# Kernel optimization log

Measured on AMD Instinct MI355X. Metric: run time of the kernel, lower is better.

## Reference

```python
import jax, jax.numpy as jnp
import numpy as np

B, N, D, H = 4, 1024, 1024, 16
DH = D // H
MLP = 4 * D
EPS = 1e-6


def setup_inputs() -> dict:
    key = jax.random.key(0)
    ks = jax.random.split(key, 16)
    s = lambda fan_in: 1.0 / np.sqrt(fan_in)
    inp = {
        "x": jax.random.normal(ks[0], (B, N, D), jnp.float32),
        "c": jax.random.normal(ks[1], (B, D), jnp.float32),
        # weights stored (in, out); torch Linear is x @ W.T + b
        "Wq": jax.random.normal(ks[2], (D, D), jnp.float32) * s(D),
        "bq": jnp.zeros((D,), jnp.float32),
        "Wkv": jax.random.normal(ks[3], (D, 2 * D), jnp.float32) * s(D),
        "bkv": jnp.zeros((2 * D,), jnp.float32),
        "Wo": jax.random.normal(ks[4], (D, D), jnp.float32) * s(D),
        "bo": jnp.zeros((D,), jnp.float32),
        "W1": jax.random.normal(ks[5], (D, MLP), jnp.float32) * s(D),
        "b1": jnp.zeros((MLP,), jnp.float32),
        "W2": jax.random.normal(ks[6], (MLP, D), jnp.float32) * s(MLP),
        "b2": jnp.zeros((D,), jnp.float32),
        "Wada": jax.random.normal(ks[7], (D, 6 * D), jnp.float32) * s(D),
        "bada": jnp.zeros((6 * D,), jnp.float32),
    }
    return inp


def _layernorm(h):
    mu = jnp.mean(h, axis=-1, keepdims=True)
    var = jnp.mean(jnp.square(h - mu), axis=-1, keepdims=True)
    return (h - mu) / jnp.sqrt(var + EPS)


def _modulate(h, shift, scale):
    return h * (1.0 + scale[:, None, :]) + shift[:, None, :]


def reference(x, c, Wq, bq, Wkv, bkv, Wo, bo, W1, b1, W2, b2, Wada, bada):
    scale = DH ** -0.5
    mod = jax.nn.silu(c) @ Wada + bada  # [B, 6D]
    sh_msa, sc_msa, g_msa, sh_mlp, sc_mlp, g_mlp = jnp.split(mod, 6, axis=-1)

    # --- attention branch ---
    h = _modulate(_layernorm(x), sh_msa, sc_msa)
    q = (h @ Wq + bq).reshape(B, N, H, DH)
    kv = h @ Wkv + bkv
    k, v = jnp.split(kv, 2, axis=-1)
    k = k.reshape(B, N, H, DH)
    v = v.reshape(B, N, H, DH)
    sim = jnp.einsum("bihd,bjhd->bhij", q, k) * scale  # [B,H,N,N]
    attn = jax.nn.softmax(sim, axis=-1)
    out = jnp.einsum("bhij,bjhd->bihd", attn, v).reshape(B, N, D)
    out = out @ Wo + bo
    x = x + g_msa[:, None, :] * out

    # --- MLP branch ---
    h2 = _modulate(_layernorm(x), sh_mlp, sc_mlp)
    m = jax.nn.gelu(h2 @ W1 + b1, approximate=True) @ W2 + b2
    x = x + g_mlp[:, None, :] * m
    return x
```

## Files before the change

kernel.cpp:

```cpp
#include <hip/hip_runtime.h>
#include <hip/hip_bf16.h>
#include <cstdint>

typedef __attribute__((ext_vector_type(4))) float f32x4;
typedef __attribute__((ext_vector_type(16))) float f32x16;
typedef __attribute__((ext_vector_type(8))) short s16x8;
typedef __attribute__((ext_vector_type(4))) unsigned u32x4;
typedef unsigned short u16;

#define B_  4
#define N_  1024
#define D_  1024
#define H_  16
#define DH_ 64
#define M_  4096
#define SIXD 6144

#define WAITV(n) asm volatile("s_waitcnt vmcnt(" #n ")" ::: "memory")

__device__ __forceinline__ u16 f2bf(float f) {
    unsigned u = __builtin_bit_cast(unsigned, f);
    unsigned r = (u + 0x7fffu + ((u >> 16) & 1u)) >> 16;
    return (u16)r;
}

__device__ __forceinline__ unsigned cvtpk(float a, float b) {
    unsigned r;
    asm("v_cvt_pk_bf16_f32 %0, %1, %2" : "=v"(r) : "v"(a), "v"(b));
    return r;
}

__device__ __forceinline__ void gload16(const void* g, void* l) {
    __builtin_amdgcn_global_load_lds((const __attribute__((address_space(1))) void*)g,
                                     (__attribute__((address_space(3))) void*)l,
                                     16, 0, 0);
}

__global__ __launch_bounds__(256) void prep_all(const float* __restrict__ Wq,
                                                const float* __restrict__ Wkv,
                                                const float* __restrict__ Wo,
                                                const float* __restrict__ W1,
                                                const float* __restrict__ W2,
                                                const float* __restrict__ c,
                                                const float* __restrict__ Wada,
                                                const float* __restrict__ bada,
                                                u16* __restrict__ wqkvT,
                                                u16* __restrict__ woT,
                                                u16* __restrict__ w1T,
                                                u16* __restrict__ w2T,
                                                float* __restrict__ mod) {
    int id = blockIdx.x;
    int tid = threadIdx.x;
    if (id >= 12288) {
        __shared__ float sc[D_];
        int mb = id - 12288;
        int b = mb / 24;
        int col = (mb % 24) * 256 + tid;
        for (int i = tid; i < D_; i += 256) {
            float v = c[b * D_ + i];
            sc[i] = v / (1.f + __expf(-v));
        }
        __syncthreads();
        float a0 = 0.f, a1 = 0.f, a2 = 0.f, a3 = 0.f;
        for (int k = 0; k < D_; k += 4) {
            a0 = fmaf(sc[k + 0], Wada[(size_t)(k + 0) * SIXD + col], a0);
            a1 = fmaf(sc[k + 1], Wada[(size_t)(k + 1) * SIXD + col], a1);
            a2 = fmaf(sc[k + 2], Wada[(size_t)(k + 2) * SIXD + col], a2);
            a3 = fmaf(sc[k + 3], Wada[(size_t)(k + 3) * SIXD + col], a3);
        }
        mod[b * SIXD + col] = bada[col] + ((a0 + a1) + (a2 + a3));
        return;
    }
    const float* in; u16* outp; int R, C, loc;
    if (id < 1024)      { in = Wq;  outp = wqkvT;           R = 1024; C = 1024; loc = id; }
    else if (id < 3072) { in = Wkv; outp = wqkvT + 1048576; R = 1024; C = 2048; loc = id - 1024; }
    else if (id < 4096) { in = Wo;  outp = woT;             R = 1024; C = 1024; loc = id - 3072; }
    else if (id < 8192) { in = W1;  outp = w1T;             R = 1024; C = 4096; loc = id - 4096; }
    else                { in = W2;  outp = w2T;             R = 4096; C = 1024; loc = id - 8192; }
    int tpc = C >> 5;
    int bx = loc % tpc, by = loc / tpc;
    __shared__ float t[32][33];
    int tx = tid & 31, ty = tid >> 5;
    int r0 = by * 32, c0 = bx * 32;
#pragma unroll
    for (int i = 0; i < 4; ++i)
        t[ty + 8 * i][tx] = in[(size_t)(r0 + ty + 8 * i) * C + c0 + tx];
    __syncthreads();
#pragma unroll
    for (int i = 0; i < 4; ++i)
        outp[(size_t)(c0 + ty + 8 * i) * R + r0 + tx] = f2bf(t[tx][ty + 8 * i]);
}

__global__ __launch_bounds__(256) void ln_mod(const float* __restrict__ x,
                                              const float* __restrict__ mod,
                                              int shift_c, int scale_c,
                                              u16* __restrict__ h) {
    int row = blockIdx.x;
    int b = row >> 10;
    int tid = threadIdx.x, w = tid >> 6;
    float4 xv = ((const float4*)(x + (size_t)row * D_))[tid];
    float s  = xv.x + xv.y + xv.z + xv.w;
    float s2 = xv.x * xv.x + xv.y * xv.y + xv.z * xv.z + xv.w * xv.w;
#pragma unroll
    for (int m = 1; m <= 32; m <<= 1) { s += __shfl_xor(s, m); s2 += __shfl_xor(s2, m); }
    __shared__ float red[8];
    if ((tid & 63) == 0) { red[w * 2] = s; red[w * 2 + 1] = s2; }
    __syncthreads();
    float S  = red[0] + red[2] + red[4] + red[6];
    float S2 = red[1] + red[3] + red[5] + red[7];
    float mu = S * (1.f / D_);
    float var = S2 * (1.f / D_) - mu * mu;
    float rstd = rsqrtf(var + 1e-6f);
    int d0 = tid * 4;
    float4 shv = *(const float4*)(mod + b * SIXD + shift_c * D_ + d0);
    float4 scv = *(const float4*)(mod + b * SIXD + scale_c * D_ + d0);
    ushort4 o;
    o.x = f2bf((xv.x - mu) * rstd * (1.f + scv.x) + shv.x);
    o.y = f2bf((xv.y - mu) * rstd * (1.f + scv.y) + shv.y);
    o.z = f2bf((xv.z - mu) * rstd * (1.f + scv.z) + shv.z);
    o.w = f2bf((xv.w - mu) * rstd * (1.f + scv.w) + shv.w);
    *(ushort4*)(h + (size_t)row * D_ + d0) = o;
}

__global__ __launch_bounds__(256) void gemm_qkv(const u16* __restrict__ A,
                                                const u16* __restrict__ Bt,
                                                const float* __restrict__ bias,
                                                const float* __restrict__ bias2,
                                                u16* __restrict__ out,
                                                int M, int Nn, int K) {
    __shared__ char lds[2][32768];
    const int tid = threadIdx.x;
    const int w = tid >> 6, lane = tid & 63;
    const int li = lane & 15, lg = lane >> 4;
    const int nwg = gridDim.x * gridDim.y;
    const int flat = blockIdx.y * gridDim.x + blockIdx.x;
    const int wg = (flat & 7) * (nwg >> 3) + (flat >> 3);
    const int m0 = (wg / gridDim.x) * 128, n0 = (wg % gridDim.x) * 128;
    const int wr = w >> 1, wc = w & 1;

    f32x4 acc[4][4];
#pragma unroll
    for (int i = 0; i < 4; ++i)
#pragma unroll
        for (int j = 0; j < 4; ++j) acc[i][j] = (f32x4){0.f, 0.f, 0.f, 0.f};

    auto STAGE = [&](int kk, char* buf) {
#pragma unroll
        for (int j = 0; j < 8; ++j) {
            int basec = j * 256 + w * 64;
            int idx = basec + lane;
            int idl = idx & 1023;
            int row = idl >> 3, cc = idl & 7;
            const u16* src;
            if (idx < 1024)
                src = A + (size_t)(m0 + row) * K + kk + ((cc ^ (row & 7)) << 3);
            else
                src = Bt + (size_t)(n0 + row) * K + kk + ((cc ^ (row & 7)) << 3);
            gload16(src, buf + basec * 16);
        }
    };

    const int nt = K >> 6;
    STAGE(0, lds[0]);
    __syncthreads();
    int cur = 0;
    for (int t = 0; t < nt; ++t) {
        if (t + 1 < nt) { STAGE((t + 1) << 6, lds[cur ^ 1]); WAITV(8); }
        else WAITV(0);
        __builtin_amdgcn_s_barrier();
        __builtin_amdgcn_sched_barrier(0);
        const char* Ab = lds[cur];
        const char* Bb = lds[cur] + 16384;
#pragma unroll
        for (int hh = 0; hh < 2; ++hh) {
            s16x8 af[4], bfr[4];
#pragma unroll
            for (int mi = 0; mi < 4; ++mi) {
                int r = wr * 64 + mi * 16 + li;
                af[mi] = *(const s16x8*)(Ab + r * 128 + (((hh * 4 + lg) ^ (r & 7)) << 4));
            }
#pragma unroll
            for (int nj = 0; nj < 4; ++nj) {
                int r = wc * 64 + nj * 16 + li;
                bfr[nj] = *(const s16x8*)(Bb + r * 128 + (((hh * 4 + lg) ^ (r & 7)) << 4));
            }
#pragma unroll
            for (int mi = 0; mi < 4; ++mi)
#pragma unroll
                for (int nj = 0; nj < 4; ++nj)
                    acc[mi][nj] = __builtin_amdgcn_mfma_f32_16x16x32_bf16(
                        af[mi], bfr[nj], acc[mi][nj], 0, 0, 0);
        }
        __builtin_amdgcn_s_barrier();
        cur ^= 1;
    }

#pragma unroll
    for (int mi = 0; mi < 4; ++mi) {
#pragma unroll
        for (int nj = 0; nj < 4; ++nj) {
            int col = n0 + wc * 64 + nj * 16 + li;
            float bv = (col < D_) ? bias[col] : bias2[col - D_];
#pragma unroll
            for (int rg = 0; rg < 4; ++rg) {
                int grow = m0 + wr * 64 + mi * 16 + 4 * lg + rg;
                float v = acc[mi][nj][rg] + bv;
                int b = grow >> 10, n = grow & 1023;
                if (col < D_) {
                    int hd = col >> 6, dh = col & 63;
                    out[(((size_t)(b * H_ + hd)) * N_ + n) * DH_ + dh] = f2bf(v);
                } else if (col < 2 * D_) {
                    int c2 = col - D_;
                    int hd = c2 >> 6, dh = c2 & 63;
                    out[4194304u + (((size_t)(b * H_ + hd)) * N_ + n) * DH_ + dh] = f2bf(v);
                } else {
                    int c2 = col - 2 * D_;
                    int hd = c2 >> 6, dh = c2 & 63;
                    out[8388608u + (((size_t)(b * H_ + hd)) * DH_ + dh) * N_ + n] = f2bf(v);
                }
            }
        }
    }
}

template <int EPI>
__global__ __launch_bounds__(256) void gemm_bt(const u16* __restrict__ A,
                                               const u16* __restrict__ Bt,
                                               const float* __restrict__ bias,
                                               void* __restrict__ out,
                                               const float* __restrict__ xres,
                                               const float* __restrict__ mod,
                                               int M, int Nn, int K, int gate_c) {
    __shared__ char lds[2][32768];
    const int tid = threadIdx.x;
    const int w = tid >> 6, lane = tid & 63;
    const int li = lane & 15, lg = lane >> 4;
    const int nwg = gridDim.x * gridDim.y;
    const int flat = blockIdx.y * gridDim.x + blockIdx.x;
    const int wg = (flat & 7) * (nwg >> 3) + (flat >> 3);
    const int m0 = (wg / gridDim.x) * 128, n0 = (wg % gridDim.x) * 128;
    const int wr = w >> 1, wc = w & 1;

    f32x4 acc[4][4];
#pragma unroll
    for (int i = 0; i < 4; ++i)
#pragma unroll
        for (int j = 0; j < 4; ++j) acc[i][j] = (f32x4){0.f, 0.f, 0.f, 0.f};

    auto STAGE = [&](int kk, char* buf) {
#pragma unroll
        for (int j = 0; j < 8; ++j) {
            int basec = j * 256 + w * 64;
            int idx = basec + lane;
            int idl = idx & 1023;
            int row = idl >> 3, cc = idl & 7;
            const u16* src;
            if (idx < 1024)
                src = A + (size_t)(m0 + row) * K + kk + ((cc ^ (row & 7)) << 3);
            else
                src = Bt + (size_t)(n0 + row) * K + kk + ((cc ^ (row & 7)) << 3);
            gload16(src, buf + basec * 16);
        }
    };

    const int nt = K >> 6;
    STAGE(0, lds[0]);
    __syncthreads();
    int cur = 0;
    for (int t = 0; t < nt; ++t) {
        if (t + 1 < nt) { STAGE((t + 1) << 6, lds[cur ^ 1]); WAITV(8); }
        else WAITV(0);
        __builtin_amdgcn_s_barrier();
        __builtin_amdgcn_sched_barrier(0);
        const char* Ab = lds[cur];
        const char* Bb = lds[cur] + 16384;
#pragma unroll
        for (int hh = 0; hh < 2; ++hh) {
            s16x8 af[4], bfr[4];
#pragma unroll
            for (int mi = 0; mi < 4; ++mi) {
                int r = wr * 64 + mi * 16 + li;
                af[mi] = *(const s16x8*)(Ab + r * 128 + (((hh * 4 + lg) ^ (r & 7)) << 4));
            }
#pragma unroll
            for (int nj = 0; nj < 4; ++nj) {
                int r = wc * 64 + nj * 16 + li;
                bfr[nj] = *(const s16x8*)(Bb + r * 128 + (((hh * 4 + lg) ^ (r & 7)) << 4));
            }
#pragma unroll
            for (int mi = 0; mi < 4; ++mi)
#pragma unroll
                for (int nj = 0; nj < 4; ++nj)
                    acc[mi][nj] = __builtin_amdgcn_mfma_f32_16x16x32_bf16(
                        af[mi], bfr[nj], acc[mi][nj], 0, 0, 0);
        }
        __builtin_amdgcn_s_barrier();
        cur ^= 1;
    }

#pragma unroll
    for (int mi = 0; mi < 4; ++mi) {
#pragma unroll
        for (int nj = 0; nj < 4; ++nj) {
            int col = n0 + wc * 64 + nj * 16 + li;
            float bv = bias[col];
#pragma unroll
            for (int rg = 0; rg < 4; ++rg) {
                int grow = m0 + wr * 64 + mi * 16 + 4 * lg + rg;
                float v = acc[mi][nj][rg] + bv;
                int b = grow >> 10;
                size_t off = (size_t)grow * D_ + col;
                float g = mod[b * SIXD + gate_c * D_ + col];
                ((float*)out)[off] = xres[off] + g * v;
            }
        }
    }
}

__global__ __launch_bounds__(512, 2) void gemm256_gelu(const u16* __restrict__ A,
                                                       const u16* __restrict__ Bt,
                                                       const float* __restrict__ bias,
                                                       u16* __restrict__ out,
                                                       int M, int Nn, int K) {
    __shared__ char lds[2][65536];
    const int tid = threadIdx.x;
    const int w = tid >> 6, lane = tid & 63;
    const int li = lane & 15, lg = lane >> 4;
    const int wr = w >> 1, wc = w & 1;

    const int flat = blockIdx.x;
    const int wg = (flat & 7) * 32 + (flat >> 3);
    const int mg = wg >> 6, r_ = wg & 63;
    const int mt = mg * 4 + (r_ & 3), nt_ = r_ >> 2;
    const int m0 = mt * 256, n0 = nt_ * 256;

    f32x4 acc[4][8];
#pragma unroll
    for (int i = 0; i < 4; ++i)
#pragma unroll
        for (int j = 0; j < 8; ++j) acc[i][j] = (f32x4){0.f, 0.f, 0.f, 0.f};

    auto STAGE = [&](int kk, char* buf) {
#pragma unroll
        for (int j = 0; j < 4; ++j) {
            int basec = j * 512 + w * 64;
            int idx = basec + lane;
            int row = idx >> 3, cc = idx & 7;
            gload16(A + (size_t)(m0 + row) * K + kk + ((cc ^ (row & 7)) << 3),
                    buf + basec * 16);
            gload16(Bt + (size_t)(n0 + row) * K + kk + ((cc ^ (row & 7)) << 3),
                    buf + 32768 + basec * 16);
        }
    };

    const int nt = K >> 6;
    STAGE(0, lds[0]);
    __syncthreads();
    int cur = 0;
    for (int t = 0; t < nt; ++t) {
        if (t + 1 < nt) STAGE((t + 1) << 6, lds[cur ^ 1]);
        const char* Ab = lds[cur];
        const char* Bb = lds[cur] + 32768;
#pragma unroll
        for (int hh = 0; hh < 2; ++hh) {
            s16x8 af[4], bfr[8];
#pragma unroll
            for (int mi = 0; mi < 4; ++mi) {
                int r = wr * 64 + mi * 16 + li;
                af[mi] = *(const s16x8*)(Ab + r * 128 + (((hh * 4 + lg) ^ (r & 7)) << 4));
            }
#pragma unroll
            for (int nj = 0; nj < 8; ++nj) {
                int r = wc * 128 + nj * 16 + li;
                bfr[nj] = *(const s16x8*)(Bb + r * 128 + (((hh * 4 + lg) ^ (r & 7)) << 4));
            }
#pragma unroll
            for (int mi = 0; mi < 4; ++mi)
#pragma unroll
                for (int nj = 0; nj < 8; ++nj)
                    acc[mi][nj] = __builtin_amdgcn_mfma_f32_16x16x32_bf16(
                        af[mi], bfr[nj], acc[mi][nj], 0, 0, 0);
        }
        __syncthreads();
        cur ^= 1;
    }

#pragma unroll
    for (int nj = 0; nj < 8; ++nj) {
        int col = n0 + wc * 128 + nj * 16 + li;
        float bv = bias[col];
#pragma unroll
        for (int mi = 0; mi < 4; ++mi) {
#pragma unroll
            for (int rg = 0; rg < 4; ++rg) {
                int grow = m0 + wr * 64 + mi * 16 + 4 * lg + rg;
                float v = acc[mi][nj][rg] + bv;
                float u = 0.7978845608028654f * v * (1.f + 0.044715f * v * v);
                u = fminf(fmaxf(u, -15.f), 15.f);
                float e = __expf(2.f * u);
                float th = (e - 1.f) / (e + 1.f);
                out[(size_t)grow * (size_t)Nn + col] = f2bf(0.5f * v * (1.f + th));
            }
        }
    }
}

__global__ __launch_bounds__(256) void attn2(const u16* __restrict__ q,
                                             const u16* __restrict__ k,
                                             const u16* __restrict__ vt,
                                             u16* __restrict__ o) {
    __shared__ __align__(16) char qs[16384];
    __shared__ __align__(16) char kv[2][16384];
    const int tid = threadIdx.x, w = tid >> 6, lane = tid & 63;
    const int l31 = lane & 31, hi = lane >> 5;
    const int flat = blockIdx.x;
    const int wgs = (flat & 7) * 64 + (flat >> 3);
    const int bh = wgs >> 3, qt = wgs & 7;
    const size_t base = (size_t)bh * (N_ * DH_);
    const int q0 = qt * 128;

#pragma unroll
    for (int j = 0; j < 4; ++j) {
        int basec = j * 256 + w * 64;
        int idx = basec + lane;
        int row = idx >> 3, cc = idx & 7;
        gload16(q + base + (size_t)(q0 + row) * DH_ + ((cc ^ (row & 7)) << 3),
                qs + basec * 16);
    }
    auto STAGEKV = [&](int t, char* buf) {
#pragma unroll
        for (int j = 0; j < 4; ++j) {
            int basec = j * 256 + w * 64;
            int idx = basec + lane;
            if (idx < 512) {
                int row = idx >> 3, cc = idx & 7;
                gload16(k + base + (size_t)(t * 64 + row) * DH_ + ((cc ^ (row & 7)) << 3),
                        buf + basec * 16);
            } else {
                int i2 = idx - 512;
                int row = i2 >> 3, cc = i2 & 7;
                gload16(vt + base + (size_t)row * N_ + t * 64 + ((cc ^ (row & 7)) << 3),
                        buf + basec * 16);
            }
        }
    };
    STAGEKV(0, kv[0]);
    __syncthreads();

    s16x8 qf[4];
    const int qr = w * 32 + l31;
#pragma unroll
    for (int st = 0; st < 4; ++st)
        qf[st] = *(const s16x8*)(qs + qr * 128 + (((st * 2 + hi) ^ (qr & 7)) << 4));

    f32x16 oa[2];
#pragma unroll
    for (int r = 0; r < 16; ++r) { oa[0][r] = 0.f; oa[1][r] = 0.f; }
    float mrow = -3e38f, lrow = 0.f;
    const float CSC = 0.125f * 1.44269504088896f;

    int cur = 0;
    for (int t = 0; t < 16; ++t) {
        if (t + 1 < 16) STAGEKV(t + 1, kv[cur ^ 1]);
        const char* Kb = kv[cur];
        const char* Vb = kv[cur] + 8192;

        f32x16 s[2];
#pragma unroll
        for (int r = 0; r < 16; ++r) { s[0][r] = 0.f; s[1][r] = 0.f; }
#pragma unroll
        for (int st = 0; st < 4; ++st) {
#pragma unroll
            for (int ks = 0; ks < 2; ++ks) {
                int r = ks * 32 + l31;
                s16x8 ka = *(const s16x8*)(Kb + r * 128 + (((st * 2 + hi) ^ (r & 7)) << 4));
                s[ks] = __builtin_amdgcn_mfma_f32_32x32x16_bf16(ka, qf[st], s[ks], 0, 0, 0);
            }
        }

        float tmax = s[0][0];
#pragma unroll
        for (int r = 1; r < 16; ++r) tmax = fmaxf(tmax, s[0][r]);
#pragma unroll
        for (int r = 0; r < 16; ++r) tmax = fmaxf(tmax, s[1][r]);
        tmax = fmaxf(tmax, __shfl_xor(tmax, 32));
        float mn = fmaxf(mrow, tmax);
        float al = __builtin_amdgcn_exp2f((mrow - mn) * CSC);
        float nmc = -mn * CSC;
        float rs0 = 0.f, rs1 = 0.f;
#pragma unroll
        for (int r = 0; r < 16; ++r) {
            float p0 = __builtin_amdgcn_exp2f(fmaf(s[0][r], CSC, nmc));
            float p1 = __builtin_amdgcn_exp2f(fmaf(s[1][r], CSC, nmc));
            s[0][r] = p0; s[1][r] = p1;
            rs0 += p0; rs1 += p1;
        }
        float rs = rs0 + rs1;
        rs += __shfl_xor(rs, 32);
        lrow = lrow * al + rs;
        mrow = mn;
#pragma unroll
        for (int r = 0; r < 16; ++r) { oa[0][r] *= al; oa[1][r] *= al; }

        unsigned u[16];
#pragma unroll
        for (int ks = 0; ks < 2; ++ks)
#pragma unroll
            for (int j = 0; j < 4; ++j) {
                u[ks * 8 + 2 * j]     = cvtpk(s[ks][4 * j + 0], s[ks][4 * j + 1]);
                u[ks * 8 + 2 * j + 1] = cvtpk(s[ks][4 * j + 2], s[ks][4 * j + 3]);
            }

#pragma unroll
        for (int kstep = 0; kstep < 4; ++kstep) {
            unsigned b0 = u[kstep * 4 + 0], b1 = u[kstep * 4 + 1];
            unsigned b2 = u[kstep * 4 + 2], b3 = u[kstep * 4 + 3];
            asm volatile("v_permlane32_swap_b32 %0, %1" : "+v"(b0), "+v"(b2));
            asm volatile("v_permlane32_swap_b32 %0, %1" : "+v"(b1), "+v"(b3));
            u32x4 pbu = (u32x4){b0, b1, b2, b3};
            s16x8 pb = __builtin_bit_cast(s16x8, pbu);
#pragma unroll
            for (int ds = 0; ds < 2; ++ds) {
                int r = ds * 32 + l31;
                s16x8 va = *(const s16x8*)(Vb + r * 128 + (((kstep * 2 + hi) ^ (r & 7)) << 4));
                oa[ds] = __builtin_amdgcn_mfma_f32_32x32x16_bf16(va, pb, oa[ds], 0, 0, 0);
            }
        }
        __syncthreads();
        cur ^= 1;
    }

    float inv = 1.f / lrow;
#pragma unroll
    for (int ds = 0; ds < 2; ++ds)
#pragma unroll
        for (int j = 0; j < 4; ++j)
#pragma unroll
            for (int t2 = 0; t2 < 2; ++t2) {
                unsigned pk = cvtpk(oa[ds][4 * j + 2 * t2] * inv,
                                    oa[ds][4 * j + 2 * t2 + 1] * inv);
                int row = qr;
                int dch = 4 * ds + j;
                *(unsigned*)(qs + row * 128 + ((dch ^ (row & 7)) << 4) +
                             (4 * hi + 2 * t2) * 2) = pk;
            }
    __syncthreads();
    {
        int r = tid >> 1, h2 = tid & 1;
        const int b = bh >> 4, hd = bh & 15;
        size_t obase = ((size_t)(b * N_ + q0 + r)) * D_ + hd * DH_;
#pragma unroll
        for (int c = 0; c < 4; ++c) {
            int c2 = h2 * 4 + c;
            s16x8 v = *(const s16x8*)(qs + r * 128 + ((c2 ^ (r & 7)) << 4));
            *(s16x8*)(o + obase + c2 * 8) = v;
        }
    }
}

extern "C" void kernel_launch(void* const* d_in, const int* in_sizes, int n_in,
                              void* d_out, int out_size, void* d_ws, size_t ws_size,
                              hipStream_t stream) {
    const float* x    = (const float*)d_in[0];
    const float* c    = (const float*)d_in[1];
    const float* Wq   = (const float*)d_in[2];
    const float* bq   = (const float*)d_in[3];
    const float* Wkv  = (const float*)d_in[4];
    const float* bkv  = (const float*)d_in[5];
    const float* Wo   = (const float*)d_in[6];
    const float* bo   = (const float*)d_in[7];
    const float* W1   = (const float*)d_in[8];
    const float* b1   = (const float*)d_in[9];
    const float* W2   = (const float*)d_in[10];
    const float* b2   = (const float*)d_in[11];
    const float* Wada = (const float*)d_in[12];
    const float* bada = (const float*)d_in[13];

    char* ws = (char*)d_ws;
    const size_t MB = 1024 * 1024;
    u16*   wqkvT = (u16*)(ws + 0);
    u16*   woT  = (u16*)(ws + 6 * MB);
    u16*   w1T  = (u16*)(ws + 8 * MB);
    u16*   w2T  = (u16*)(ws + 16 * MB);
    float* mod  = (float*)(ws + 24 * MB);
    u16*   h    = (u16*)(ws + 25 * MB);
    u16*   qb   = (u16*)(ws + 33 * MB);
    u16*   ao   = (u16*)(ws + 57 * MB);
    float* x1   = (float*)(ws + 65 * MB);
    u16*   m1   = (u16*)(ws + 33 * MB);
    float* outp = (float*)d_out;

    prep_all<<<12384, 256, 0, stream>>>(Wq, Wkv, Wo, W1, W2, c, Wada, bada,
                                        wqkvT, woT, w1T, w2T, mod);

    ln_mod<<<M_, 256, 0, stream>>>(x, mod, 0, 1, h);

    gemm_qkv<<<dim3(24, 32), 256, 0, stream>>>(h, wqkvT, bq, bkv, qb, M_, 3 * D_, D_);

    attn2<<<512, 256, 0, stream>>>(qb, qb + 4194304, qb + 8388608, ao);

    gemm_bt<2><<<dim3(8, 32), 256, 0, stream>>>(ao, woT, bo, x1, x, mod, M_, D_, D_, 2);

    ln_mod<<<M_, 256, 0, stream>>>(x1, mod, 3, 4, h);

    gemm256_gelu<<<256, 512, 0, stream>>>(h, w1T, b1, m1, M_, 4 * D_, D_);
    gemm_bt<4><<<dim3(8, 32), 256, 0, stream>>>(m1, w2T, b2, outp, x1, mod, M_, D_, 4 * D_, 5);
}
```

Measured before the change: 242.0 us.

## Split adaLN modulation GEMV over K and enlarge weight transpose tiles

```diff
diff --git a/kernel.cpp b/kernel.cpp
--- a/kernel.cpp
+++ b/kernel.cpp
@@ -43,52 +43,69 @@
                                                 const float* __restrict__ W2,
                                                 const float* __restrict__ c,
                                                 const float* __restrict__ Wada,
-                                                const float* __restrict__ bada,
                                                 u16* __restrict__ wqkvT,
                                                 u16* __restrict__ woT,
                                                 u16* __restrict__ w1T,
                                                 u16* __restrict__ w2T,
-                                                float* __restrict__ mod) {
+                                                float* __restrict__ modp) {
     int id = blockIdx.x;
     int tid = threadIdx.x;
-    if (id >= 12288) {
-        __shared__ float sc[D_];
-        int mb = id - 12288;
-        int b = mb / 24;
-        int col = (mb % 24) * 256 + tid;
-        for (int i = tid; i < D_; i += 256) {
-            float v = c[b * D_ + i];
-            sc[i] = v / (1.f + __expf(-v));
+    if (id < 768) {
+        __shared__ float sc[128];
+        int colblk = id % 24, b = (id / 24) & 3, ks = id / 96;
+        int col = colblk * 256 + tid;
+        int k0 = ks * 128;
+        if (tid < 128) {
+            float v = c[b * D_ + k0 + tid];
+            sc[tid] = v / (1.f + __expf(-v));
         }
         __syncthreads();
         float a0 = 0.f, a1 = 0.f, a2 = 0.f, a3 = 0.f;
-        for (int k = 0; k < D_; k += 4) {
-            a0 = fmaf(sc[k + 0], Wada[(size_t)(k + 0) * SIXD + col], a0);
-            a1 = fmaf(sc[k + 1], Wada[(size_t)(k + 1) * SIXD + col], a1);
-            a2 = fmaf(sc[k + 2], Wada[(size_t)(k + 2) * SIXD + col], a2);
-            a3 = fmaf(sc[k + 3], Wada[(size_t)(k + 3) * SIXD + col], a3);
-        }
-        mod[b * SIXD + col] = bada[col] + ((a0 + a1) + (a2 + a3));
+#pragma unroll 4
+        for (int k = 0; k < 128; k += 4) {
+            a0 = fmaf(sc[k + 0], Wada[(size_t)(k0 + k + 0) * SIXD + col], a0);
+            a1 = fmaf(sc[k + 1], Wada[(size_t)(k0 + k + 1) * SIXD + col], a1);
+            a2 = fmaf(sc[k + 2], Wada[(size_t)(k0 + k + 2) * SIXD + col], a2);
+            a3 = fmaf(sc[k + 3], Wada[(size_t)(k0 + k + 3) * SIXD + col], a3);
+        }
+        modp[(size_t)(ks * 4 + b) * SIXD + col] = (a0 + a1) + (a2 + a3);
         return;
     }
+    int t_ = id - 768;
     const float* in; u16* outp; int R, C, loc;
-    if (id < 1024)      { in = Wq;  outp = wqkvT;           R = 1024; C = 1024; loc = id; }
-    else if (id < 3072) { in = Wkv; outp = wqkvT + 1048576; R = 1024; C = 2048; loc = id - 1024; }
-    else if (id < 4096) { in = Wo;  outp = woT;             R = 1024; C = 1024; loc = id - 3072; }
-    else if (id < 8192) { in = W1;  outp = w1T;             R = 1024; C = 4096; loc = id - 4096; }
-    else                { in = W2;  outp = w2T;             R = 4096; C = 1024; loc = id - 8192; }
-    int tpc = C >> 5;
+    if (t_ < 256)       { in = Wq;  outp = wqkvT;           R = 1024; C = 1024; loc = t_; }
+    else if (t_ < 768)  { in = Wkv; outp = wqkvT + 1048576; R = 1024; C = 2048; loc = t_ - 256; }
+    else if (t_ < 1024) { in = Wo;  outp = woT;             R = 1024; C = 1024; loc = t_ - 768; }
+    else if (t_ < 2048) { in = W1;  outp = w1T;             R = 1024; C = 4096; loc = t_ - 1024; }
+    else                { in = W2;  outp = w2T;             R = 4096; C = 1024; loc = t_ - 2048; }
+    int tpc = C >> 6;
     int bx = loc % tpc, by = loc / tpc;
-    __shared__ float t[32][33];
-    int tx = tid & 31, ty = tid >> 5;
-    int r0 = by * 32, c0 = bx * 32;
-#pragma unroll
-    for (int i = 0; i < 4; ++i)
-        t[ty + 8 * i][tx] = in[(size_t)(r0 + ty + 8 * i) * C + c0 + tx];
+    __shared__ float t[64][65];
+    int r0 = by * 64, c0 = bx * 64;
+    int cx = tid & 63, ry = tid >> 6;
+#pragma unroll
+    for (int i = 0; i < 16; ++i) {
+        int rr = ry + 4 * i;
+        t[rr][cx] = in[(size_t)(r0 + rr) * C + c0 + cx];
+    }
     __syncthreads();
 #pragma unroll
-    for (int i = 0; i < 4; ++i)
-        outp[(size_t)(c0 + ty + 8 * i) * R + r0 + tx] = f2bf(t[tx][ty + 8 * i]);
+    for (int i = 0; i < 16; ++i) {
+        int cc = ry + 4 * i;
+        outp[(size_t)(c0 + cc) * R + r0 + cx] = f2bf(t[cx][cc]);
+    }
+}
+
+__global__ __launch_bounds__(256) void reduce_mod(const float* __restrict__ modp,
+                                                  const float* __restrict__ bada,
+                                                  float* __restrict__ mod) {
+    int col = blockIdx.x * 256 + threadIdx.x;
+    int b = blockIdx.y;
+    float s = bada[col];
+#pragma unroll
+    for (int ks = 0; ks < 8; ++ks)
+        s += modp[(size_t)(ks * 4 + b) * SIXD + col];
+    mod[b * SIXD + col] = s;
 }
 
 __global__ __launch_bounds__(256) void ln_mod(const float* __restrict__ x,
@@ -583,6 +600,7 @@
     u16*   w1T  = (u16*)(ws + 8 * MB);
     u16*   w2T  = (u16*)(ws + 16 * MB);
     float* mod  = (float*)(ws + 24 * MB);
+    float* modp = (float*)(ws + 24 * MB + 131072);
     u16*   h    = (u16*)(ws + 25 * MB);
     u16*   qb   = (u16*)(ws + 33 * MB);
     u16*   ao   = (u16*)(ws + 57 * MB);
@@ -590,8 +608,9 @@
     u16*   m1   = (u16*)(ws + 33 * MB);
     float* outp = (float*)d_out;
 
-    prep_all<<<12384, 256, 0, stream>>>(Wq, Wkv, Wo, W1, W2, c, Wada, bada,
-                                        wqkvT, woT, w1T, w2T, mod);
+    prep_all<<<3840, 256, 0, stream>>>(Wq, Wkv, Wo, W1, W2, c, Wada,
+                                       wqkvT, woT, w1T, w2T, modp);
+    reduce_mod<<<dim3(24, 4), 256, 0, stream>>>(modp, bada, mod);
 
     ln_mod<<<M_, 256, 0, stream>>>(x, mod, 0, 1, h);
 
```

Result: faster. 220.6 us (-8.9%).
